# Performance work log

Hardware: AMD Instinct MI355X
Metric: run time of the kernel (lower is better)

## Reference

```python
import jax, jax.numpy as jnp
from jax import lax
import numpy as np

B, C, T = 16, 512, 4096
COEFF_INIT = 0.04


def setup_inputs() -> dict:
    key = jax.random.key(0)
    k1, k2 = jax.random.split(key)
    x = jax.random.normal(k1, (B, C, T), dtype=jnp.float32)
    # learned per-channel smoothing coefficients, initialized like the module
    weights = jnp.ones((C,), dtype=jnp.float32) * COEFF_INIT
    return {"x": x, "weights": weights}


def reference(x, weights):
    # clamp weights to [0, 1] (mirrors the in-place no-grad clamp; values stay
    # unchanged here since coeff_init is inside the range)
    s = jnp.clip(weights, 0.0, 1.0)  # [C]
    xt = jnp.moveaxis(x, 2, 0)       # [T, B, C]
    init = xt[0]                      # y_0 = x_0

    def step(acc, sample):
        acc = s * sample + (1.0 - s) * acc
        return acc, acc

    _, ys = lax.scan(step, init, xt[1:])          # [T-1, B, C]
    out = jnp.concatenate([init[None], ys], axis=0)  # [T, B, C]
    return jnp.moveaxis(out, 0, 2)                   # [B, C, T]
```

## Files before the change

kernel.cpp:

```cpp
#include <hip/hip_runtime.h>


constexpr int T_LEN = 4096;
constexpr int C_LEN = 512;
constexpr int WAVES_PER_BLOCK = 4;
constexpr int BLOCK = 64 * WAVES_PER_BLOCK;
constexpr int CHUNKS = 16;

__global__ __launch_bounds__(BLOCK, 4) void ema_wave_kernel(
    const float* __restrict__ x,
    const float* __restrict__ w,
    float* __restrict__ y)
{
    const int wave = threadIdx.x >> 6;
    const int lane = threadIdx.x & 63;
    const int row  = blockIdx.x * WAVES_PER_BLOCK + wave;
    const int c    = row & (C_LEN - 1);

    float s = w[c];
    s = fminf(fmaxf(s, 0.0f), 1.0f);
    const float a = 1.0f - s;

    const float4* xp = (const float4*)(x + (size_t)row * T_LEN);
    float4*       yp = (float4*)(y + (size_t)row * T_LEN);

    float4 v[CHUNKS];
    #pragma unroll
    for (int k = 0; k < CHUNKS; ++k)
        v[k] = xp[(k << 6) + lane];

    const float a2 = a * a, a3 = a2 * a, a4 = a2 * a2;

    float S[CHUNKS];
    #pragma unroll
    for (int k = 0; k < CHUNKS; ++k) {
        float l0 = s * v[k].x;
        if (k == 0 && lane == 0) l0 = v[0].x;
        float l1 = fmaf(a, l0, s * v[k].y);
        float l2 = fmaf(a, l1, s * v[k].z);
        float l3 = fmaf(a, l2, s * v[k].w);
        v[k].x = l0; v[k].y = l1; v[k].z = l2; v[k].w = l3;
        S[k] = l3;
    }

    float wgt = a4;
    #pragma unroll
    for (int d = 1; d < 64; d <<= 1) {
        #pragma unroll
        for (int k = 0; k < CHUNKS; ++k) {
            float up = __shfl_up(S[k], d, 64);
            if (lane >= d) S[k] = fmaf(wgt, up, S[k]);
        }
        wgt *= wgt;
    }
    const float a256 = wgt;

    float powl = 1.0f, tq = a4;
    #pragma unroll
    for (int b = 0; b < 6; ++b) {
        if ((lane >> b) & 1) powl *= tq;
        tq *= tq;
    }

    float Ek = 0.0f;
    #pragma unroll
    for (int k = 0; k < CHUNKS; ++k) {
        float Sx = __shfl_up(S[k], 1, 64);
        float base = (lane == 0) ? 0.0f : Sx;
        float P = fmaf(powl, Ek, base);
        float4 o;
        o.x = fmaf(a,  P, v[k].x);
        o.y = fmaf(a2, P, v[k].y);
        o.z = fmaf(a3, P, v[k].z);
        o.w = fmaf(a4, P, v[k].w);
        yp[(k << 6) + lane] = o;

        float Tk = __shfl(S[k], 63, 64);
        Ek = fmaf(a256, Ek, Tk);
    }
}

extern "C" void kernel_launch(void* const* d_in, const int* in_sizes, int n_in,
                              void* d_out, int out_size, void* d_ws, size_t ws_size,
                              hipStream_t stream) {
    const float* x = (const float*)d_in[0];
    const float* w = (const float*)d_in[1];
    float* y = (float*)d_out;

    const int rows = out_size / T_LEN;
    const int grid = rows / WAVES_PER_BLOCK;
    ema_wave_kernel<<<grid, BLOCK, 0, stream>>>(x, w, y);
}
```

Baseline: 235.4 us.

## Split each row across a block of four waves with shared-memory carry scan

Each block now handles one row, with four waves each scanning interleaved 256-element chunks. Chunk totals are combined across waves through shared memory and a barrier instead of a serial per-wave carry chain. Each thread now holds 4 float4 chunks instead of 16, which cuts register pressure and shortens the dependent shuffle chains. Output stores use nontemporal hints, and the cost is a __syncthreads per block plus a small redundant serial loop over 16 totals.

```diff
diff --git a/kernel.cpp b/kernel.cpp
--- a/kernel.cpp
+++ b/kernel.cpp
@@ -3,39 +3,42 @@
 
 constexpr int T_LEN = 4096;
 constexpr int C_LEN = 512;
-constexpr int WAVES_PER_BLOCK = 4;
-constexpr int BLOCK = 64 * WAVES_PER_BLOCK;
-constexpr int CHUNKS = 16;
+constexpr int BLOCK = 256;
+constexpr int NW    = 4;
+constexpr int CH    = 4;
 
-__global__ __launch_bounds__(BLOCK, 4) void ema_wave_kernel(
+typedef float nfloat4 __attribute__((ext_vector_type(4)));
+
+__global__ __launch_bounds__(BLOCK) void ema_scan_kernel(
     const float* __restrict__ x,
     const float* __restrict__ w,
     float* __restrict__ y)
 {
-    const int wave = threadIdx.x >> 6;
-    const int lane = threadIdx.x & 63;
-    const int row  = blockIdx.x * WAVES_PER_BLOCK + wave;
+    const int row  = blockIdx.x;
     const int c    = row & (C_LEN - 1);
+    const int tid  = threadIdx.x;
+    const int lane = tid & 63;
+    const int wv   = tid >> 6;
 
     float s = w[c];
     s = fminf(fmaxf(s, 0.0f), 1.0f);
     const float a = 1.0f - s;
 
-    const float4* xp = (const float4*)(x + (size_t)row * T_LEN);
-    float4*       yp = (float4*)(y + (size_t)row * T_LEN);
+    const nfloat4* xp = (const nfloat4*)(x + (size_t)row * T_LEN);
+    nfloat4*       yp = (nfloat4*)(y + (size_t)row * T_LEN);
 
-    float4 v[CHUNKS];
+    nfloat4 v[CH];
     #pragma unroll
-    for (int k = 0; k < CHUNKS; ++k)
-        v[k] = xp[(k << 6) + lane];
+    for (int k = 0; k < CH; ++k)
+        v[k] = xp[(k << 8) + (wv << 6) + lane];
 
     const float a2 = a * a, a3 = a2 * a, a4 = a2 * a2;
 
-    float S[CHUNKS];
+    float S[CH];
     #pragma unroll
-    for (int k = 0; k < CHUNKS; ++k) {
+    for (int k = 0; k < CH; ++k) {
         float l0 = s * v[k].x;
-        if (k == 0 && lane == 0) l0 = v[0].x;
+        if (k == 0 && tid == 0) l0 = v[0].x;
         float l1 = fmaf(a, l0, s * v[k].y);
         float l2 = fmaf(a, l1, s * v[k].z);
         float l3 = fmaf(a, l2, s * v[k].w);
@@ -47,13 +50,30 @@
     #pragma unroll
     for (int d = 1; d < 64; d <<= 1) {
         #pragma unroll
-        for (int k = 0; k < CHUNKS; ++k) {
+        for (int k = 0; k < CH; ++k) {
             float up = __shfl_up(S[k], d, 64);
             if (lane >= d) S[k] = fmaf(wgt, up, S[k]);
         }
         wgt *= wgt;
     }
     const float a256 = wgt;
+
+    __shared__ float tot[CH * NW];
+    if (lane == 63) {
+        #pragma unroll
+        for (int k = 0; k < CH; ++k) tot[(k << 2) + wv] = S[k];
+    }
+    __syncthreads();
+
+    float E[CH];
+    {
+        float R = 0.0f;
+        #pragma unroll
+        for (int m = 0; m < CH * NW; ++m) {
+            if ((m & 3) == wv) E[m >> 2] = R;
+            R = fmaf(a256, R, tot[m]);
+        }
+    }
 
     float powl = 1.0f, tq = a4;
     #pragma unroll
@@ -62,21 +82,17 @@
         tq *= tq;
     }
 
-    float Ek = 0.0f;
     #pragma unroll
-    for (int k = 0; k < CHUNKS; ++k) {
-        float Sx = __shfl_up(S[k], 1, 64);
+    for (int k = 0; k < CH; ++k) {
+        float Sx   = __shfl_up(S[k], 1, 64);
         float base = (lane == 0) ? 0.0f : Sx;
-        float P = fmaf(powl, Ek, base);
-        float4 o;
+        float P    = fmaf(powl, E[k], base);
+        nfloat4 o;
         o.x = fmaf(a,  P, v[k].x);
         o.y = fmaf(a2, P, v[k].y);
         o.z = fmaf(a3, P, v[k].z);
         o.w = fmaf(a4, P, v[k].w);
-        yp[(k << 6) + lane] = o;
-
-        float Tk = __shfl(S[k], 63, 64);
-        Ek = fmaf(a256, Ek, Tk);
+        __builtin_nontemporal_store(o, &yp[(k << 8) + (wv << 6) + lane]);
     }
 }
 
@@ -88,6 +104,5 @@
     float* y = (float*)d_out;
 
     const int rows = out_size / T_LEN;
-    const int grid = rows / WAVES_PER_BLOCK;
-    ema_wave_kernel<<<grid, BLOCK, 0, stream>>>(x, w, y);
+    ema_scan_kernel<<<rows, BLOCK, 0, stream>>>(x, w, y);
 }
```

Result: faster. 221.4 us (-5.9%).
